# Kernel tuning notes

Hardware: AMD Instinct MI355X
Metric: run time of the kernel (lower is better)

Reference implementation:

```python
import jax, jax.numpy as jnp
import numpy as np

B, W, D, R = 8, 1024, 1024, 64
GAMMA_MIN, GAMMA_MAX, ALPHA_CAP, EPS = 0.15, 1.0, 1.0, 1e-8


def _linear_init(key, fan_in, shape):
    bound = 1.0 / np.sqrt(fan_in)
    return jax.random.uniform(key, shape, jnp.float32, -bound, bound)


def setup_inputs() -> dict:
    key = jax.random.key(0)
    ks = jax.random.split(key, 12)
    h = jax.random.normal(ks[0], (B, W, D), jnp.float32)
    # k_base init as in __init__: exp(-0.15*max(j-i,0)) * tril, row-normalized
    pos = jnp.arange(W, dtype=jnp.float32)
    dist_ji = jnp.clip(pos[None, :] - pos[:, None], 0.0)
    causal = jnp.tril(jnp.ones((W, W), jnp.float32))
    k_init = jnp.exp(-0.15 * dist_ji) * causal
    k_base = k_init / jnp.clip(k_init.sum(axis=1, keepdims=True), 1e-8)
    # decay_logit init: gammas in [0.95, 0.995] -> inverse sigmoid of normalized gamma
    gammas = jnp.linspace(0.95, 0.995, R)
    graw = jnp.clip((gammas - GAMMA_MIN) / (GAMMA_MAX - GAMMA_MIN), 1e-6, 1 - 1e-6)
    decay_logit = jnp.log(graw / (1.0 - graw))
    return {
        "h": h,
        "k_base": k_base,
        "decay_logit": decay_logit,
        "gate_logit": jnp.asarray(8.0, jnp.float32),
        "alpha_logit": jnp.asarray(0.0, jnp.float32),
        "u": 0.05 * jax.random.normal(ks[1], (D, R), jnp.float32),
        "v": 0.05 * jax.random.normal(ks[2], (D, R), jnp.float32),
        "proj_w": _linear_init(ks[3], D, (D, D)),
        "proj_b": _linear_init(ks[4], D, (D,)),
        "norm1_scale": jnp.ones((D,), jnp.float32),
        "norm2_scale": jnp.ones((D,), jnp.float32),
        "up_w": _linear_init(ks[5], D, (2 * D, D)),
        "up_b": _linear_init(ks[6], D, (2 * D,)),
        "down_w": _linear_init(ks[7], 2 * D, (D, 2 * D)),
        "down_b": _linear_init(ks[8], 2 * D, (D,)),
    }


def _rmsnorm(x, scale):
    return x * jax.lax.rsqrt(jnp.mean(x * x, axis=-1, keepdims=True) + 1e-8) * scale


def _l2norm(x):
    # mirrors F.normalize(x, dim=-1, eps=1e-8)
    n = jnp.sqrt(jnp.sum(x * x, axis=-1, keepdims=True))
    return x / jnp.maximum(n, EPS)


def reference(h, k_base, decay_logit, gate_logit, alpha_logit, u, v,
              proj_w, proj_b, norm1_scale, norm2_scale,
              up_w, up_b, down_w, down_b):
    _, w, _ = h.shape
    pos = jnp.arange(w, dtype=h.dtype)
    causal = jnp.tril(jnp.ones((w, w), h.dtype))          # [W, W]
    dist = jnp.clip(pos[:, None] - pos[None, :], 0.0)     # i - j, clamped >= 0

    residual = h
    h_norm = _rmsnorm(h, norm1_scale)

    # dense k_base path (k_base_rank == 0)
    gate = jax.nn.sigmoid(gate_logit)
    kb = k_base[:w, :w] * causal
    out = gate * jnp.einsum('ij,bjd->bid', kb, h_norm)

    # low-rank q/k with per-rank gamma decay (decay_impl='mask')
    qk = h_norm @ jnp.concatenate((u, v), axis=1)          # [B, W, 2R]
    q_raw, k_raw = jnp.split(qk, [u.shape[1]], axis=-1)
    q = _l2norm(q_raw)
    k = _l2norm(k_raw)

    gamma = GAMMA_MIN + (GAMMA_MAX - GAMMA_MIN) * jax.nn.sigmoid(decay_logit)  # [R]
    log_gamma = jnp.log(jnp.clip(gamma, 1e-8))
    decay_mask = jnp.exp(dist[:, :, None] * log_gamma[None, None, :]) * causal[:, :, None]  # [W, W, R]

    alpha = ALPHA_CAP * jax.nn.sigmoid(alpha_logit)
    # scores[b,i,j] = sum_r q[b,i,r] * decay[i,j,r] * k[b,j,r]
    scores = jnp.einsum('bir,ijr,bjr->bij', q, decay_mask, k)
    out = out + alpha * jnp.einsum('bij,bjd->bid', scores, h_norm)

    h1 = residual + (out @ proj_w.T + proj_b)
    # MLP (GELU exact, mult=2), second residual
    m = _rmsnorm(h1, norm2_scale)
    m = jax.nn.gelu(m @ up_w.T + up_b, approximate=False) @ down_w.T + down_b
    return h1 + m
```

## Files before the change

### kernel.cpp

```cpp
#include <hip/hip_runtime.h>
#include <hip/hip_bf16.h>
#include <math.h>

#define B_ 8
#define W_ 1024
#define D_ 1024
#define R_ 64

typedef __hip_bfloat16 bf16;
typedef __attribute__((ext_vector_type(8))) short bf16x8;
typedef __attribute__((ext_vector_type(4))) float f32x4;

__device__ __forceinline__ float tof(bf16 x) { return __bfloat162float(x); }
__device__ __forceinline__ short f2bs(float f) {
    bf16 b = __float2bfloat16(f);
    return *(short*)&b;
}

__device__ __forceinline__ void async16(const void* g, void* l) {
    __builtin_amdgcn_global_load_lds(
        (const __attribute__((address_space(1))) unsigned int*)g,
        (__attribute__((address_space(3))) unsigned int*)l,
        16, 0, 0);
}

__global__ __launch_bounds__(256)
void rmsnorm_kernel(const float* __restrict__ src, const float* __restrict__ scale,
                    bf16* __restrict__ dst) {
    int row = blockIdx.x;
    const float* x = src + (size_t)row * D_;
    bf16* y = dst + (size_t)row * D_;
    float xv[4];
    float ss = 0.f;
#pragma unroll
    for (int it = 0; it < 4; ++it) {
        int d = threadIdx.x + it * 256;
        xv[it] = x[d];
        ss += xv[it] * xv[it];
    }
#pragma unroll
    for (int off = 32; off; off >>= 1) ss += __shfl_down(ss, off, 64);
    __shared__ float red[4];
    __shared__ float invs;
    int lane = threadIdx.x & 63, wid = threadIdx.x >> 6;
    if (lane == 0) red[wid] = ss;
    __syncthreads();
    if (threadIdx.x == 0) {
        float t = red[0] + red[1] + red[2] + red[3];
        invs = rsqrtf(t / (float)D_ + 1e-8f);
    }
    __syncthreads();
    float inv = invs;
#pragma unroll
    for (int it = 0; it < 4; ++it) {
        int d = threadIdx.x + it * 256;
        y[d] = __float2bfloat16(xv[it] * inv * scale[d]);
    }
}

__global__ __launch_bounds__(256)
void transpose_kernel(const bf16* __restrict__ src, bf16* __restrict__ dst) {
    int b = blockIdx.z;
    int j0 = blockIdx.x * 64, d0 = blockIdx.y * 64;
    __shared__ short Ts[64][72];
    const bf16* S = src + (size_t)b * W_ * D_;
    bf16* Dd = dst + (size_t)b * W_ * D_;
    int tid = threadIdx.x;
    int r = tid >> 3, c = (tid & 7) * 8;
#pragma unroll
    for (int p = 0; p < 2; ++p) {
        int j = r + p * 32;
        bf16x8 vv = *(const bf16x8*)&S[(size_t)(j0 + j) * D_ + d0 + c];
#pragma unroll
        for (int e = 0; e < 8; ++e) Ts[j][c + e] = vv[e];
    }
    __syncthreads();
#pragma unroll
    for (int p = 0; p < 2; ++p) {
        int d = r + p * 32;
        bf16x8 vv;
#pragma unroll
        for (int e = 0; e < 8; ++e) vv[e] = Ts[c + e][d];
        *(bf16x8*)&Dd[(size_t)(d0 + d) * W_ + j0 + c] = vv;
    }
}

__global__ __launch_bounds__(256)
void uvT_kernel(const float* __restrict__ u, const float* __restrict__ v,
                bf16* __restrict__ uvT) {
    int g = blockIdx.z;
    int d0 = blockIdx.x * 64;
    const float* src = g ? v : u;
    __shared__ float Ts[64][65];
    int tid = threadIdx.x;
#pragma unroll
    for (int e = 0; e < 16; ++e) {
        int idx = tid + e * 256;
        int drow = idx >> 6, rcol = idx & 63;
        Ts[drow][rcol] = src[(size_t)(d0 + drow) * 64 + rcol];
    }
    __syncthreads();
#pragma unroll
    for (int e = 0; e < 16; ++e) {
        int idx = tid + e * 256;
        int orow = idx >> 6, ocol = idx & 63;
        uvT[(size_t)(g * 64 + orow) * D_ + d0 + ocol] = __float2bfloat16(Ts[ocol][orow]);
    }
}

__global__ __launch_bounds__(256)
void convert3_kernel(const float* __restrict__ proj, const float* __restrict__ up,
                     const float* __restrict__ down,
                     bf16* __restrict__ projb, bf16* __restrict__ upb,
                     bf16* __restrict__ downb) {
    size_t idx = ((size_t)blockIdx.x * 256 + threadIdx.x) * 8;
    const size_t DD = (size_t)D_ * D_;
    const float* src; bf16* dst; size_t off;
    if (idx < DD)          { src = proj; dst = projb; off = idx; }
    else if (idx < 3 * DD) { src = up;   dst = upb;   off = idx - DD; }
    else                   { src = down; dst = downb; off = idx - 3 * DD; }
    float4 f0 = *(const float4*)(src + off);
    float4 f1 = *(const float4*)(src + off + 4);
    bf16x8 p;
    p[0] = f2bs(f0.x); p[1] = f2bs(f0.y); p[2] = f2bs(f0.z); p[3] = f2bs(f0.w);
    p[4] = f2bs(f1.x); p[5] = f2bs(f1.y); p[6] = f2bs(f1.z); p[7] = f2bs(f1.w);
    *(bf16x8*)(dst + off) = p;
}

__global__ __launch_bounds__(128)
void qk_epilogue_kernel(const float* __restrict__ qkraw,
                        const float* __restrict__ decay_logit,
                        float* __restrict__ qg, float* __restrict__ kg) {
    int row = blockIdx.x;
    int i = row & (W_ - 1);
    int t = threadIdx.x;
    int r = t & 63;
    bool isK = t >= 64;
    const size_t PS = (size_t)B_ * W_ * 128;
    size_t off = (size_t)row * 128 + t;
    float val = qkraw[off] + qkraw[PS + off] + qkraw[2 * PS + off] + qkraw[3 * PS + off];
    float sq = val * val;
#pragma unroll
    for (int o = 32; o; o >>= 1) sq += __shfl_xor(sq, o, 64);
    val = val / fmaxf(sqrtf(sq), 1e-8f);

    float dl = decay_logit[r];
    float gamma = 0.15f + 0.85f * (1.f / (1.f + expf(-dl)));
    float lg = logf(gamma);
    float e = isK ? expf(-(float)i * lg) : expf((float)i * lg);
    float o = val * e;
    if (isK) kg[(size_t)row * R_ + r] = o;
    else     qg[(size_t)row * R_ + r] = o;
}

__global__ __launch_bounds__(256)
void buildM_kernel(const float* __restrict__ qg, const float* __restrict__ kg,
                   const float* __restrict__ k_base,
                   const float* __restrict__ gate_logit,
                   const float* __restrict__ alpha_logit,
                   bf16* __restrict__ M) {
    int b = blockIdx.z;
    int ti = blockIdx.y, tj = blockIdx.x;
    int i0 = ti * 32, j0 = tj * 32;
    int tx = threadIdx.x, ty = threadIdx.y;
    bf16* Mb = M + (size_t)b * W_ * W_;
    const bf16 zero = __float2bfloat16(0.f);

    if (tj > ti) {
#pragma unroll
        for (int a = 0; a < 2; ++a)
#pragma unroll
            for (int c = 0; c < 2; ++c)
                Mb[(size_t)(i0 + ty * 2 + a) * W_ + (j0 + tx * 2 + c)] = zero;
        return;
    }

    __shared__ float Qs[32][65];
    __shared__ float Ks[32][65];
    int tid = ty * 16 + tx;
    for (int e = tid; e < 32 * 64; e += 256) {
        int rr = e & 63, row = e >> 6;
        Qs[row][rr] = qg[((size_t)b * W_ + i0 + row) * R_ + rr];
        Ks[row][rr] = kg[((size_t)b * W_ + j0 + row) * R_ + rr];
    }
    __syncthreads();

    float acc[2][2] = {{0.f, 0.f}, {0.f, 0.f}};
#pragma unroll 8
    for (int r = 0; r < 64; ++r) {
        float qa = Qs[ty * 2 + 0][r], qb = Qs[ty * 2 + 1][r];
        float ka = Ks[tx * 2 + 0][r], kb = Ks[tx * 2 + 1][r];
        acc[0][0] += qa * ka; acc[0][1] += qa * kb;
        acc[1][0] += qb * ka; acc[1][1] += qb * kb;
    }

    float gate  = 1.f / (1.f + expf(-(*gate_logit)));
    float alpha = 1.f / (1.f + expf(-(*alpha_logit)));
#pragma unroll
    for (int a = 0; a < 2; ++a) {
#pragma unroll
        for (int c = 0; c < 2; ++c) {
            int i = i0 + ty * 2 + a, j = j0 + tx * 2 + c;
            float vkb = k_base[(size_t)i * W_ + j];
            float out = (j <= i) ? (gate * vkb + alpha * acc[a][c]) : 0.f;
            Mb[(size_t)i * W_ + j] = __float2bfloat16(out);
        }
    }
}

#define BAR() do { __builtin_amdgcn_sched_barrier(0); \
                   __builtin_amdgcn_s_barrier(); \
                   __builtin_amdgcn_sched_barrier(0); } while (0)

__device__ __forceinline__ void mfma8(const bf16x8 (&fa)[2], const bf16x8 (&fb)[4],
                                      f32x4 (&acc)[2][4]) {
#pragma unroll
    for (int mi = 0; mi < 2; ++mi)
#pragma unroll
        for (int ni = 0; ni < 4; ++ni)
            acc[mi][ni] = __builtin_amdgcn_mfma_f32_16x16x32_bf16(
                fa[mi], fb[ni], acc[mi][ni], 0, 0, 0);
}

__device__ __forceinline__ void readf(const short* At0, const short* Bt0, int slot,
                                      const int (&ao)[2], const int (&bo)[4],
                                      bf16x8 (&fa)[2], bf16x8 (&fb)[4]) {
    const short* Ard = At0 + slot * 4096;
    const short* Brd = Bt0 + slot * 4096;
#pragma unroll
    for (int mi = 0; mi < 2; ++mi) fa[mi] = *(const bf16x8*)&Ard[ao[mi]];
#pragma unroll
    for (int ni = 0; ni < 4; ++ni) fb[ni] = *(const bf16x8*)&Brd[bo[ni]];
}

template<int EPI, int SK>
__global__ __launch_bounds__(512, 4)
void mgemm_kernel(const bf16* __restrict__ A, const bf16* __restrict__ Bm,
                  const float* __restrict__ Res, const float* __restrict__ bias,
                  void* __restrict__ Cout,
                  int M, int N, int K,
                  long sA, long sB, long sC, int causal) {
    __shared__ __align__(16) short At[5][128 * 32];
    __shared__ __align__(16) short Bt[5][128 * 32];
    int z = blockIdx.z;
    const bf16* Ab = (SK > 1) ? A : A + (size_t)z * sA;
    const bf16* Bb = (SK > 1) ? Bm : Bm + (size_t)z * sB;
    int kchunk = K / SK;
    int kbeg = (SK > 1) ? z * kchunk : 0;
    int m0 = blockIdx.x * 128, n0 = blockIdx.y * 128;
    int tid = threadIdx.x;
    int lane = tid & 63, wave = tid >> 6;
    int wy = wave >> 1, wx = wave & 1;
    int quad = lane >> 4, l15 = lane & 15;

    f32x4 acc[2][4];
#pragma unroll
    for (int i = 0; i < 2; ++i)
#pragma unroll
        for (int j = 0; j < 4; ++j)
            acc[i][j] = (f32x4){0.f, 0.f, 0.f, 0.f};

    int kend = kbeg + kchunk;
    if (SK == 1 && causal) kend = (m0 + 128 < K) ? m0 + 128 : K;
    int nIter = (kend - kbeg) >> 5;

    int srcChunk = ((lane & 3) ^ ((lane >> 3) & 3)) * 8;
    size_t rowA = (size_t)(m0 + wave * 16 + (lane >> 2)) * K;
    size_t rowB = (size_t)(n0 + wave * 16 + (lane >> 2)) * K;
    const bf16* aP = Ab + rowA + srcChunk + kbeg;
    const bf16* bP = Bb + rowB + srcChunk + kbeg;
    short* aDst = &At[0][0] + wave * 512;
    short* bDst = &Bt[0][0] + wave * 512;

    int rswz = (quad ^ ((l15 >> 1) & 3)) * 8;
    int ao[2], bo[4];
#pragma unroll
    for (int mi = 0; mi < 2; ++mi) ao[mi] = (wy * 32 + mi * 16 + l15) * 32 + rswz;
#pragma unroll
    for (int ni = 0; ni < 4; ++ni) bo[ni] = (wx * 64 + ni * 16 + l15) * 32 + rswz;

#pragma unroll
    for (int p = 0; p < 4; ++p) {
        async16(aP, aDst + p * 4096);
        async16(bP, bDst + p * 4096);
        aP += 32; bP += 32;
    }
    asm volatile("s_waitcnt vmcnt(6)" ::: "memory");
    BAR();

    bf16x8 fa0[2], fb0[4], fa1[2], fb1[4];
    readf(&At[0][0], &Bt[0][0], 0, ao, bo, fa0, fb0);

    int sStage = 4;
    int sPf = 1;
    int nMain = nIter - 4;

    for (int t = 0; t < nMain; t += 2) {
        asm volatile("s_waitcnt vmcnt(4)" ::: "memory");
        BAR();
        async16(aP, aDst + sStage * 4096);
        async16(bP, bDst + sStage * 4096);
        aP += 32; bP += 32;
        sStage = (sStage == 4) ? 0 : sStage + 1;
        mfma8(fa0, fb0, acc);
        readf(&At[0][0], &Bt[0][0], sPf, ao, bo, fa1, fb1);
        sPf = (sPf == 4) ? 0 : sPf + 1;
        asm volatile("s_waitcnt vmcnt(4)" ::: "memory");
        BAR();
        async16(aP, aDst + sStage * 4096);
        async16(bP, bDst + sStage * 4096);
        aP += 32; bP += 32;
        sStage = (sStage == 4) ? 0 : sStage + 1;
        mfma8(fa1, fb1, acc);
        readf(&At[0][0], &Bt[0][0], sPf, ao, bo, fa0, fb0);
        sPf = (sPf == 4) ? 0 : sPf + 1;
    }

    asm volatile("s_waitcnt vmcnt(4)" ::: "memory");
    BAR();
    mfma8(fa0, fb0, acc);
    readf(&At[0][0], &Bt[0][0], sPf, ao, bo, fa1, fb1);
    sPf = (sPf == 4) ? 0 : sPf + 1;

    asm volatile("s_waitcnt vmcnt(2)" ::: "memory");
    BAR();
    mfma8(fa1, fb1, acc);
    readf(&At[0][0], &Bt[0][0], sPf, ao, bo, fa0, fb0);
    sPf = (sPf == 4) ? 0 : sPf + 1;

    asm volatile("s_waitcnt vmcnt(0)" ::: "memory");
    BAR();
    mfma8(fa0, fb0, acc);
    readf(&At[0][0], &Bt[0][0], sPf, ao, bo, fa1, fb1);

    mfma8(fa1, fb1, acc);

#pragma unroll
    for (int ni = 0; ni < 4; ++ni) {
        int col = n0 + wx * 64 + ni * 16 + l15;
        float bv = (EPI == 1 || EPI == 2) ? bias[col] : 0.f;
#pragma unroll
        for (int mi = 0; mi < 2; ++mi) {
            int row0 = m0 + wy * 32 + mi * 16 + quad * 4;
#pragma unroll
            for (int r = 0; r < 4; ++r) {
                size_t idx = (size_t)(row0 + r) * N + col;
                float val = acc[mi][ni][r];
                if constexpr (EPI == 0) {
                    ((bf16*)Cout)[(size_t)z * sC + idx] = __float2bfloat16(val);
                } else if constexpr (EPI == 1) {
                    ((float*)Cout)[idx] = val + bv + Res[idx];
                } else if constexpr (EPI == 2) {
                    val += bv;
                    val = 0.5f * val * (1.f + erff(val * 0.70710678118654752f));
                    ((bf16*)Cout)[idx] = __float2bfloat16(val);
                } else {
                    ((float*)Cout)[(size_t)z * sC + idx] = val;
                }
            }
        }
    }
}

extern "C" void kernel_launch(void* const* d_in, const int* in_sizes, int n_in,
                              void* d_out, int out_size, void* d_ws, size_t ws_size,
                              hipStream_t stream) {
    const float* h           = (const float*)d_in[0];
    const float* k_base      = (const float*)d_in[1];
    const float* decay_logit = (const float*)d_in[2];
    const float* gate_logit  = (const float*)d_in[3];
    const float* alpha_logit = (const float*)d_in[4];
    const float* u           = (const float*)d_in[5];
    const float* v           = (const float*)d_in[6];
    const float* proj_w      = (const float*)d_in[7];
    const float* proj_b      = (const float*)d_in[8];
    const float* norm1_scale = (const float*)d_in[9];
    const float* norm2_scale = (const float*)d_in[10];
    const float* up_w        = (const float*)d_in[11];
    const float* up_b        = (const float*)d_in[12];
    const float* down_w      = (const float*)d_in[13];
    const float* down_b      = (const float*)d_in[14];

    const size_t MB = 1048576;
    char* ws = (char*)d_ws;
    bf16*  hnorm   = (bf16*)(ws);
    bf16*  uvT     = (bf16*)(ws + 16 * MB);
    float* qg      = (float*)(ws + 16 * MB);
    float* kg      = (float*)(ws + 18 * MB);
    bf16*  hnormT  = (bf16*)(ws + 20 * MB);
    float* qkraw   = (float*)(ws + 36 * MB);
    bf16*  Mbuf    = (bf16*)(ws + 36 * MB);
    bf16*  proj_wb = (bf16*)(ws + 52 * MB);
    bf16*  up_wb   = (bf16*)(ws + 54 * MB);
    bf16*  down_wb = (bf16*)(ws + 58 * MB);
    bf16*  attn    = hnorm;
    bf16*  mnorm   = hnorm;
    bf16*  tbuf    = hnormT;
    float* h1      = (float*)d_out;

    convert3_kernel<<<5 * D_ * D_ / 2048, 256, 0, stream>>>(
        proj_w, up_w, down_w, proj_wb, up_wb, down_wb);
    uvT_kernel<<<dim3(D_ / 64, 1, 2), 256, 0, stream>>>(u, v, uvT);

    rmsnorm_kernel<<<B_ * W_, 256, 0, stream>>>(h, norm1_scale, hnorm);

    transpose_kernel<<<dim3(W_ / 64, D_ / 64, B_), 256, 0, stream>>>(hnorm, hnormT);

    mgemm_kernel<5, 4><<<dim3(B_ * W_ / 128, 1, 4), 512, 0, stream>>>(
        hnorm, uvT, nullptr, nullptr, qkraw, B_ * W_, 128, D_,
        0, 0, (long)B_ * W_ * 128, 0);

    qk_epilogue_kernel<<<B_ * W_, 128, 0, stream>>>(qkraw, decay_logit, qg, kg);

    buildM_kernel<<<dim3(W_ / 32, W_ / 32, B_), dim3(16, 16), 0, stream>>>(
        qg, kg, k_base, gate_logit, alpha_logit, Mbuf);

    mgemm_kernel<0, 1><<<dim3(W_ / 128, D_ / 128, B_), 512, 0, stream>>>(
        Mbuf, hnormT, nullptr, nullptr, attn, W_, D_, W_,
        (long)W_ * W_, (long)W_ * D_, (long)W_ * D_, 1);

    mgemm_kernel<1, 1><<<dim3(B_ * W_ / 128, D_ / 128, 1), 512, 0, stream>>>(
        attn, proj_wb, h, proj_b, h1, B_ * W_, D_, D_, 0, 0, 0, 0);

    rmsnorm_kernel<<<B_ * W_, 256, 0, stream>>>(h1, norm2_scale, mnorm);

    mgemm_kernel<2, 1><<<dim3(B_ * W_ / 128, 2 * D_ / 128, 1), 512, 0, stream>>>(
        mnorm, up_wb, nullptr, up_b, tbuf, B_ * W_, 2 * D_, D_, 0, 0, 0, 0);

    mgemm_kernel<1, 1><<<dim3(B_ * W_ / 128, D_ / 128, 1), 512, 0, stream>>>(
        tbuf, down_wb, h1, down_b, (float*)d_out, B_ * W_, D_, 2 * D_, 0, 0, 0, 0);
}
```

Before: 350.1 us.

## Add 256x128-tile GEMM with triple-buffered async LDS loads for main matmuls

Introduces a new GEMM kernel using 256x128 output tiles (8 waves each computing 64x64 with 16x16x32 bf16 MFMA), a three-stage global-to-LDS async pipeline with swizzled shared layout, and an 8-way block remap for L2 locality. The attention, projection, up and down GEMMs switch to it. This is meant to raise data reuse per loaded tile and hide memory latency better. The cost is half as many blocks and more LDS per block, which can lower occupancy or leave the GPU with fewer blocks to schedule than before.

```diff
diff --git a/kernel.cpp b/kernel.cpp
--- a/kernel.cpp
+++ b/kernel.cpp
@@ -362,6 +362,131 @@
     }
 }
 
+__device__ __forceinline__ void mfma16(const bf16x8 (&fa)[4], const bf16x8 (&fb)[4],
+                                       f32x4 (&acc)[4][4]) {
+#pragma unroll
+    for (int mi = 0; mi < 4; ++mi)
+#pragma unroll
+        for (int ni = 0; ni < 4; ++ni)
+            acc[mi][ni] = __builtin_amdgcn_mfma_f32_16x16x32_bf16(
+                fa[mi], fb[ni], acc[mi][ni], 0, 0, 0);
+}
+
+template<int EPI>
+__global__ __launch_bounds__(512, 4)
+void mgemm2_kernel(const bf16* __restrict__ A, const bf16* __restrict__ Bm,
+                   const float* __restrict__ Res, const float* __restrict__ bias,
+                   void* __restrict__ Cout,
+                   int M, int N, int K, long sA, long sB, long sC, int causal) {
+    __shared__ __align__(16) short At[3][256 * 32];
+    __shared__ __align__(16) short Bt[3][128 * 32];
+    int z = blockIdx.z;
+    const bf16* Ab = A + (size_t)z * sA;
+    const bf16* Bb = Bm + (size_t)z * sB;
+
+    int bx = blockIdx.x, gx = gridDim.x;
+    if ((gx & 7) == 0) { int cpx = gx >> 3; bx = (bx & 7) * cpx + (bx >> 3); }
+    int m0 = bx * 256, n0 = blockIdx.y * 128;
+
+    int tid = threadIdx.x;
+    int lane = tid & 63, wave = tid >> 6;
+    int wm = wave >> 1, wn = wave & 1;
+    int quad = lane >> 4, l15 = lane & 15;
+
+    f32x4 acc[4][4];
+#pragma unroll
+    for (int i = 0; i < 4; ++i)
+#pragma unroll
+        for (int j = 0; j < 4; ++j)
+            acc[i][j] = (f32x4){0.f, 0.f, 0.f, 0.f};
+
+    int kend = causal ? ((m0 + 256 < K) ? m0 + 256 : K) : K;
+    int nIter = kend >> 5;
+
+    int srcChunk = ((lane & 3) ^ ((lane >> 3) & 3)) * 8;
+    size_t rowA0 = (size_t)(m0 + wave * 32 + (lane >> 2)) * K;
+    size_t rowB  = (size_t)(n0 + wave * 16 + (lane >> 2)) * K;
+    const bf16* aP0 = Ab + rowA0 + srcChunk;
+    const bf16* aP1 = aP0 + (size_t)16 * K;
+    const bf16* bP  = Bb + rowB + srcChunk;
+    short* aDst = &At[0][0] + wave * 1024;
+    short* bDst = &Bt[0][0] + wave * 512;
+
+    int rswz = (quad ^ ((l15 >> 1) & 3)) * 8;
+    int ao[4], bo[4];
+#pragma unroll
+    for (int mi = 0; mi < 4; ++mi) ao[mi] = (wm * 64 + mi * 16 + l15) * 32 + rswz;
+#pragma unroll
+    for (int ni = 0; ni < 4; ++ni) bo[ni] = (wn * 64 + ni * 16 + l15) * 32 + rswz;
+
+    async16(aP0, aDst);
+    async16(aP1, aDst + 512);
+    async16(bP,  bDst);
+    aP0 += 32; aP1 += 32; bP += 32;
+    if (nIter > 1) {
+        async16(aP0, aDst + 8192);
+        async16(aP1, aDst + 8192 + 512);
+        async16(bP,  bDst + 4096);
+        aP0 += 32; aP1 += 32; bP += 32;
+        asm volatile("s_waitcnt vmcnt(3)" ::: "memory");
+    } else {
+        asm volatile("s_waitcnt vmcnt(0)" ::: "memory");
+    }
+    BAR();
+
+    int sCur = 0;
+    int sStage = 2;
+
+    for (int t = 0; t < nIter; ++t) {
+        bool i2 = (t + 2 < nIter);
+        if (i2) {
+            async16(aP0, aDst + sStage * 8192);
+            async16(aP1, aDst + sStage * 8192 + 512);
+            async16(bP,  bDst + sStage * 4096);
+            aP0 += 32; aP1 += 32; bP += 32;
+            sStage = (sStage == 2) ? 0 : sStage + 1;
+        }
+        bf16x8 fa[4], fb[4];
+        const short* Ard = &At[0][0] + sCur * 8192;
+        const short* Brd = &Bt[0][0] + sCur * 4096;
+#pragma unroll
+        for (int mi = 0; mi < 4; ++mi) fa[mi] = *(const bf16x8*)&Ard[ao[mi]];
+#pragma unroll
+        for (int ni = 0; ni < 4; ++ni) fb[ni] = *(const bf16x8*)&Brd[bo[ni]];
+        mfma16(fa, fb, acc);
+        if (t + 1 < nIter) {
+            if (i2) asm volatile("s_waitcnt vmcnt(3)" ::: "memory");
+            else    asm volatile("s_waitcnt vmcnt(0)" ::: "memory");
+            BAR();
+            sCur = (sCur == 2) ? 0 : sCur + 1;
+        }
+    }
+
+#pragma unroll
+    for (int ni = 0; ni < 4; ++ni) {
+        int col = n0 + wn * 64 + ni * 16 + l15;
+        float bv = (EPI == 1 || EPI == 2) ? bias[col] : 0.f;
+#pragma unroll
+        for (int mi = 0; mi < 4; ++mi) {
+            int row0 = m0 + wm * 64 + mi * 16 + quad * 4;
+#pragma unroll
+            for (int r = 0; r < 4; ++r) {
+                size_t idx = (size_t)(row0 + r) * N + col;
+                float val = acc[mi][ni][r];
+                if constexpr (EPI == 0) {
+                    ((bf16*)Cout)[(size_t)z * sC + idx] = __float2bfloat16(val);
+                } else if constexpr (EPI == 1) {
+                    ((float*)Cout)[idx] = val + bv + Res[idx];
+                } else {
+                    val += bv;
+                    val = 0.5f * val * (1.f + erff(val * 0.70710678118654752f));
+                    ((bf16*)Cout)[idx] = __float2bfloat16(val);
+                }
+            }
+        }
+    }
+}
+
 extern "C" void kernel_launch(void* const* d_in, const int* in_sizes, int n_in,
                               void* d_out, int out_size, void* d_ws, size_t ws_size,
                               hipStream_t stream) {
@@ -415,18 +540,18 @@
     buildM_kernel<<<dim3(W_ / 32, W_ / 32, B_), dim3(16, 16), 0, stream>>>(
         qg, kg, k_base, gate_logit, alpha_logit, Mbuf);
 
-    mgemm_kernel<0, 1><<<dim3(W_ / 128, D_ / 128, B_), 512, 0, stream>>>(
+    mgemm2_kernel<0><<<dim3(W_ / 256, D_ / 128, B_), 512, 0, stream>>>(
         Mbuf, hnormT, nullptr, nullptr, attn, W_, D_, W_,
         (long)W_ * W_, (long)W_ * D_, (long)W_ * D_, 1);
 
-    mgemm_kernel<1, 1><<<dim3(B_ * W_ / 128, D_ / 128, 1), 512, 0, stream>>>(
+    mgemm2_kernel<1><<<dim3(B_ * W_ / 256, D_ / 128, 1), 512, 0, stream>>>(
         attn, proj_wb, h, proj_b, h1, B_ * W_, D_, D_, 0, 0, 0, 0);
 
     rmsnorm_kernel<<<B_ * W_, 256, 0, stream>>>(h1, norm2_scale, mnorm);
 
-    mgemm_kernel<2, 1><<<dim3(B_ * W_ / 128, 2 * D_ / 128, 1), 512, 0, stream>>>(
+    mgemm2_kernel<2><<<dim3(B_ * W_ / 256, 2 * D_ / 128, 1), 512, 0, stream>>>(
         mnorm, up_wb, nullptr, up_b, tbuf, B_ * W_, 2 * D_, D_, 0, 0, 0, 0);
 
-    mgemm_kernel<1, 1><<<dim3(B_ * W_ / 128, D_ / 128, 1), 512, 0, stream>>>(
+    mgemm2_kernel<1><<<dim3(B_ * W_ / 256, D_ / 128, 1), 512, 0, stream>>>(
         tbuf, down_wb, h1, down_b, (float*)d_out, B_ * W_, D_, 2 * D_, 0, 0, 0, 0);
 }
```

After: 373.4 us. 6.6% more time.

## Fuse prep kernels, vectorize rmsnorm, and retile buildM with 64x64 tiles

Applied to the files above, without the earlier changes.

Merges the weight conversion, u/v transpose and first rmsnorm into one prep kernel, cutting two launches and letting the independent work overlap. Rmsnorm now uses float4 loads and packed bf16 stores. buildM moves to 64x64 tiles with a 4x4 register micro-tile, float4 shared-memory reads and vectorized k_base loads and M stores. It also skips upper-triangular tiles that the causal GEMM presumably never reads, zeroing only the tile just above the diagonal. The risk is correctness if the downstream GEMM reads those unwritten tiles, plus added shared-memory and register pressure.

```diff
diff --git a/kernel.cpp b/kernel.cpp
--- a/kernel.cpp
+++ b/kernel.cpp
@@ -9,6 +9,7 @@
 
 typedef __hip_bfloat16 bf16;
 typedef __attribute__((ext_vector_type(8))) short bf16x8;
+typedef __attribute__((ext_vector_type(4))) short short4v;
 typedef __attribute__((ext_vector_type(4))) float f32x4;
 
 __device__ __forceinline__ float tof(bf16 x) { return __bfloat162float(x); }
@@ -24,37 +25,90 @@
         16, 0, 0);
 }
 
+__device__ __forceinline__ void rmsnorm_body(const float* __restrict__ src,
+                                             const float* __restrict__ scale,
+                                             bf16* __restrict__ dst, int row,
+                                             float* red, float* invs) {
+    const float4* x = (const float4*)(src + (size_t)row * D_);
+    bf16* y = dst + (size_t)row * D_;
+    int t = threadIdx.x;
+    float4 v = x[t];
+    float ss = v.x * v.x + v.y * v.y + v.z * v.z + v.w * v.w;
+#pragma unroll
+    for (int off = 32; off; off >>= 1) ss += __shfl_down(ss, off, 64);
+    int lane = t & 63, wid = t >> 6;
+    if (lane == 0) red[wid] = ss;
+    __syncthreads();
+    if (t == 0) {
+        float s = red[0] + red[1] + red[2] + red[3];
+        *invs = rsqrtf(s / (float)D_ + 1e-8f);
+    }
+    __syncthreads();
+    float inv = *invs;
+    float4 s4 = ((const float4*)scale)[t];
+    short4v o;
+    o[0] = f2bs(v.x * inv * s4.x);
+    o[1] = f2bs(v.y * inv * s4.y);
+    o[2] = f2bs(v.z * inv * s4.z);
+    o[3] = f2bs(v.w * inv * s4.w);
+    *(short4v*)&y[t * 4] = o;
+}
+
 __global__ __launch_bounds__(256)
 void rmsnorm_kernel(const float* __restrict__ src, const float* __restrict__ scale,
                     bf16* __restrict__ dst) {
-    int row = blockIdx.x;
-    const float* x = src + (size_t)row * D_;
-    bf16* y = dst + (size_t)row * D_;
-    float xv[4];
-    float ss = 0.f;
-#pragma unroll
-    for (int it = 0; it < 4; ++it) {
-        int d = threadIdx.x + it * 256;
-        xv[it] = x[d];
-        ss += xv[it] * xv[it];
-    }
-#pragma unroll
-    for (int off = 32; off; off >>= 1) ss += __shfl_down(ss, off, 64);
     __shared__ float red[4];
     __shared__ float invs;
-    int lane = threadIdx.x & 63, wid = threadIdx.x >> 6;
-    if (lane == 0) red[wid] = ss;
-    __syncthreads();
-    if (threadIdx.x == 0) {
-        float t = red[0] + red[1] + red[2] + red[3];
-        invs = rsqrtf(t / (float)D_ + 1e-8f);
-    }
-    __syncthreads();
-    float inv = invs;
-#pragma unroll
-    for (int it = 0; it < 4; ++it) {
-        int d = threadIdx.x + it * 256;
-        y[d] = __float2bfloat16(xv[it] * inv * scale[d]);
+    rmsnorm_body(src, scale, dst, blockIdx.x, red, &invs);
+}
+
+__global__ __launch_bounds__(256)
+void prep_kernel(const float* __restrict__ proj, const float* __restrict__ up,
+                 const float* __restrict__ down,
+                 bf16* __restrict__ projb, bf16* __restrict__ upb,
+                 bf16* __restrict__ downb,
+                 const float* __restrict__ u, const float* __restrict__ v,
+                 bf16* __restrict__ uvT,
+                 const float* __restrict__ h, const float* __restrict__ n1,
+                 bf16* __restrict__ hnorm) {
+    __shared__ float Ts[64][65];
+    __shared__ float red[4];
+    __shared__ float invs;
+    int bid = blockIdx.x;
+    int tid = threadIdx.x;
+    if (bid < 2560) {
+        size_t idx = ((size_t)bid * 256 + tid) * 8;
+        const size_t DD = (size_t)D_ * D_;
+        const float* src; bf16* dst; size_t off;
+        if (idx < DD)          { src = proj; dst = projb; off = idx; }
+        else if (idx < 3 * DD) { src = up;   dst = upb;   off = idx - DD; }
+        else                   { src = down; dst = downb; off = idx - 3 * DD; }
+        float4 f0 = *(const float4*)(src + off);
+        float4 f1 = *(const float4*)(src + off + 4);
+        bf16x8 p;
+        p[0] = f2bs(f0.x); p[1] = f2bs(f0.y); p[2] = f2bs(f0.z); p[3] = f2bs(f0.w);
+        p[4] = f2bs(f1.x); p[5] = f2bs(f1.y); p[6] = f2bs(f1.z); p[7] = f2bs(f1.w);
+        *(bf16x8*)(dst + off) = p;
+    } else if (bid < 2592) {
+        int lb = bid - 2560;
+        int g = lb >> 4;
+        int d0 = (lb & 15) * 64;
+        const float* src = g ? v : u;
+#pragma unroll
+        for (int e = 0; e < 16; ++e) {
+            int idx = tid + e * 256;
+            int drow = idx >> 6, rcol = idx & 63;
+            Ts[drow][rcol] = src[(size_t)(d0 + drow) * 64 + rcol];
+        }
+        __syncthreads();
+#pragma unroll
+        for (int e = 0; e < 16; ++e) {
+            int idx = tid + e * 256;
+            int orow = idx >> 6, ocol = idx & 63;
+            uvT[(size_t)(g * 64 + orow) * D_ + d0 + ocol] = __float2bfloat16(Ts[ocol][orow]);
+        }
+    } else {
+        rmsnorm_body(h, n1, hnorm, bid - 2592, red, &invs);
     }
 }
 
@@ -83,48 +137,6 @@
         for (int e = 0; e < 8; ++e) vv[e] = Ts[c + e][d];
         *(bf16x8*)&Dd[(size_t)(d0 + d) * W_ + j0 + c] = vv;
     }
-}
-
-__global__ __launch_bounds__(256)
-void uvT_kernel(const float* __restrict__ u, const float* __restrict__ v,
-                bf16* __restrict__ uvT) {
-    int g = blockIdx.z;
-    int d0 = blockIdx.x * 64;
-    const float* src = g ? v : u;
-    __shared__ float Ts[64][65];
-    int tid = threadIdx.x;
-#pragma unroll
-    for (int e = 0; e < 16; ++e) {
-        int idx = tid + e * 256;
-        int drow = idx >> 6, rcol = idx & 63;
-        Ts[drow][rcol] = src[(size_t)(d0 + drow) * 64 + rcol];
-    }
-    __syncthreads();
-#pragma unroll
-    for (int e = 0; e < 16; ++e) {
-        int idx = tid + e * 256;
-        int orow = idx >> 6, ocol = idx & 63;
-        uvT[(size_t)(g * 64 + orow) * D_ + d0 + ocol] = __float2bfloat16(Ts[ocol][orow]);
-    }
-}
-
-__global__ __launch_bounds__(256)
-void convert3_kernel(const float* __restrict__ proj, const float* __restrict__ up,
-                     const float* __restrict__ down,
-                     bf16* __restrict__ projb, bf16* __restrict__ upb,
-                     bf16* __restrict__ downb) {
-    size_t idx = ((size_t)blockIdx.x * 256 + threadIdx.x) * 8;
-    const size_t DD = (size_t)D_ * D_;
-    const float* src; bf16* dst; size_t off;
-    if (idx < DD)          { src = proj; dst = projb; off = idx; }
-    else if (idx < 3 * DD) { src = up;   dst = upb;   off = idx - DD; }
-    else                   { src = down; dst = downb; off = idx - 3 * DD; }
-    float4 f0 = *(const float4*)(src + off);
-    float4 f1 = *(const float4*)(src + off + 4);
-    bf16x8 p;
-    p[0] = f2bs(f0.x); p[1] = f2bs(f0.y); p[2] = f2bs(f0.z); p[3] = f2bs(f0.w);
-    p[4] = f2bs(f1.x); p[5] = f2bs(f1.y); p[6] = f2bs(f1.z); p[7] = f2bs(f1.w);
-    *(bf16x8*)(dst + off) = p;
 }
 
 __global__ __launch_bounds__(128)
@@ -161,50 +173,62 @@
                    bf16* __restrict__ M) {
     int b = blockIdx.z;
     int ti = blockIdx.y, tj = blockIdx.x;
-    int i0 = ti * 32, j0 = tj * 32;
-    int tx = threadIdx.x, ty = threadIdx.y;
+    if (tj > (ti | 1)) return;
+    int i0 = ti * 64, j0 = tj * 64;
     bf16* Mb = M + (size_t)b * W_ * W_;
-    const bf16 zero = __float2bfloat16(0.f);
+    int tid = threadIdx.x;
 
     if (tj > ti) {
-#pragma unroll
-        for (int a = 0; a < 2; ++a)
-#pragma unroll
-            for (int c = 0; c < 2; ++c)
-                Mb[(size_t)(i0 + ty * 2 + a) * W_ + (j0 + tx * 2 + c)] = zero;
+        int row = tid >> 2, c0 = (tid & 3) * 16;
+        bf16x8 z;
+#pragma unroll
+        for (int e = 0; e < 8; ++e) z[e] = 0;
+        *(bf16x8*)&Mb[(size_t)(i0 + row) * W_ + j0 + c0] = z;
+        *(bf16x8*)&Mb[(size_t)(i0 + row) * W_ + j0 + c0 + 8] = z;
         return;
     }
 
-    __shared__ float Qs[32][65];
-    __shared__ float Ks[32][65];
-    int tid = ty * 16 + tx;
-    for (int e = tid; e < 32 * 64; e += 256) {
-        int rr = e & 63, row = e >> 6;
-        Qs[row][rr] = qg[((size_t)b * W_ + i0 + row) * R_ + rr];
-        Ks[row][rr] = kg[((size_t)b * W_ + j0 + row) * R_ + rr];
+    __shared__ float Qs[64][68];
+    __shared__ float Ks[64][68];
+#pragma unroll
+    for (int e = 0; e < 4; ++e) {
+        int idx = tid + e * 256;
+        int row = idx >> 4, c4 = (idx & 15) * 4;
+        *(float4*)&Qs[row][c4] = *(const float4*)&qg[((size_t)b * W_ + i0 + row) * R_ + c4];
+        *(float4*)&Ks[row][c4] = *(const float4*)&kg[((size_t)b * W_ + j0 + row) * R_ + c4];
     }
     __syncthreads();
 
-    float acc[2][2] = {{0.f, 0.f}, {0.f, 0.f}};
-#pragma unroll 8
-    for (int r = 0; r < 64; ++r) {
-        float qa = Qs[ty * 2 + 0][r], qb = Qs[ty * 2 + 1][r];
-        float ka = Ks[tx * 2 + 0][r], kb = Ks[tx * 2 + 1][r];
-        acc[0][0] += qa * ka; acc[0][1] += qa * kb;
-        acc[1][0] += qb * ka; acc[1][1] += qb * kb;
+    int tx = tid & 15, ty = tid >> 4;
+    float acc[4][4] = {};
+#pragma unroll 4
+    for (int rq = 0; rq < 16; ++rq) {
+        float4 qa[4], kb[4];
+#pragma unroll
+        for (int a = 0; a < 4; ++a) qa[a] = *(const float4*)&Qs[ty * 4 + a][rq * 4];
+#pragma unroll
+        for (int c = 0; c < 4; ++c) kb[c] = *(const float4*)&Ks[tx * 4 + c][rq * 4];
+#pragma unroll
+        for (int a = 0; a < 4; ++a)
+#pragma unroll
+            for (int c = 0; c < 4; ++c)
+                acc[a][c] += qa[a].x * kb[c].x + qa[a].y * kb[c].y
+                           + qa[a].z * kb[c].z + qa[a].w * kb[c].w;
     }
 
     float gate  = 1.f / (1.f + expf(-(*gate_logit)));
     float alpha = 1.f / (1.f + expf(-(*alpha_logit)));
 #pragma unroll
-    for (int a = 0; a < 2; ++a) {
-#pragma unroll
-        for (int c = 0; c < 2; ++c) {
-            int i = i0 + ty * 2 + a, j = j0 + tx * 2 + c;
-            float vkb = k_base[(size_t)i * W_ + j];
-            float out = (j <= i) ? (gate * vkb + alpha * acc[a][c]) : 0.f;
-            Mb[(size_t)i * W_ + j] = __float2bfloat16(out);
-        }
+    for (int a = 0; a < 4; ++a) {
+        int i = i0 + ty * 4 + a;
+        int jb = j0 + tx * 4;
+        float4 vkb = *(const float4*)&k_base[(size_t)i * W_ + jb];
+        short4v o;
+        o[0] = (jb + 0 <= i) ? f2bs(gate * vkb.x + alpha * acc[a][0]) : (short)0;
+        o[1] = (jb + 1 <= i) ? f2bs(gate * vkb.y + alpha * acc[a][1]) : (short)0;
+        o[2] = (jb + 2 <= i) ? f2bs(gate * vkb.z + alpha * acc[a][2]) : (short)0;
+        o[3] = (jb + 3 <= i) ? f2bs(gate * vkb.w + alpha * acc[a][3]) : (short)0;
+        *(short4v*)&Mb[(size_t)i * W_ + jb] = o;
     }
 }
 
@@ -398,11 +422,9 @@
     bf16*  tbuf    = hnormT;
     float* h1      = (float*)d_out;
 
-    convert3_kernel<<<5 * D_ * D_ / 2048, 256, 0, stream>>>(
-        proj_w, up_w, down_w, proj_wb, up_wb, down_wb);
-    uvT_kernel<<<dim3(D_ / 64, 1, 2), 256, 0, stream>>>(u, v, uvT);
-
-    rmsnorm_kernel<<<B_ * W_, 256, 0, stream>>>(h, norm1_scale, hnorm);
+    prep_kernel<<<2560 + 32 + B_ * W_, 256, 0, stream>>>(
+        proj_w, up_w, down_w, proj_wb, up_wb, down_wb,
+        u, v, uvT, h, norm1_scale, hnorm);
 
     transpose_kernel<<<dim3(W_ / 64, D_ / 64, B_), 256, 0, stream>>>(hnorm, hnormT);
 
@@ -412,7 +434,7 @@
 
     qk_epilogue_kernel<<<B_ * W_, 128, 0, stream>>>(qkraw, decay_logit, qg, kg);
 
-    buildM_kernel<<<dim3(W_ / 32, W_ / 32, B_), dim3(16, 16), 0, stream>>>(
+    buildM_kernel<<<dim3(W_ / 64, W_ / 64, B_), 256, 0, stream>>>(
         qg, kg, k_base, gate_logit, alpha_logit, Mbuf);
 
     mgemm_kernel<0, 1><<<dim3(W_ / 128, D_ / 128, B_), 512, 0, stream>>>(
```

Result: faster. 329.8 us (-5.8%).
